# Performance work log

Hardware: AMD Instinct MI355X
Metric: run time of the kernel (lower is better)

Reference implementation:

```python
import jax, jax.numpy as jnp
import numpy as np

N_NODES = 50000


def gcn_conv(x, edge_index, W, b, n_nodes):
    # PyG GCNConv: add self-loops, symmetric normalization, linear, scatter-add.
    src, dst = edge_index[0], edge_index[1]
    loops = jnp.arange(n_nodes, dtype=src.dtype)
    src = jnp.concatenate([src, loops])
    dst = jnp.concatenate([dst, loops])
    # linear transform first (PyG order), reduces scatter width when out < in
    h = x @ W  # [N, out]
    deg = jax.ops.segment_sum(jnp.ones_like(dst, dtype=h.dtype), dst, num_segments=n_nodes)
    dinv = jnp.where(deg > 0, jax.lax.rsqrt(deg), 0.0)
    norm = dinv[src] * dinv[dst]  # [E+N]
    msgs = h[src] * norm[:, None]  # gather + scale, [E+N, out]
    out = jax.ops.segment_sum(msgs, dst, num_segments=n_nodes)  # scatter-add
    return out + b


def setup_inputs() -> dict:
    key = jax.random.key(0)
    k1, k2, k3, k4 = jax.random.split(key, 4)
    in_c, hid_c, out_c = 256, 128, 64
    n_edges = 800000
    features = jax.random.normal(k1, (N_NODES, in_c), dtype=jnp.float32)
    edge_index = jax.random.randint(k2, (2, n_edges), 0, N_NODES, dtype=jnp.int64)
    W1 = jax.random.normal(k3, (in_c, hid_c), dtype=jnp.float32) * (1.0 / np.sqrt(in_c))
    b1 = jnp.zeros((hid_c,), dtype=jnp.float32)
    W2 = jax.random.normal(k4, (hid_c, out_c), dtype=jnp.float32) * (1.0 / np.sqrt(hid_c))
    b2 = jnp.zeros((out_c,), dtype=jnp.float32)
    return {"features": features, "edge_index": edge_index, "W1": W1, "b1": b1, "W2": W2, "b2": b2}


def reference(features, edge_index, W1, b1, W2, b2):
    n = features.shape[0]
    x = gcn_conv(features, edge_index, W1, b1, n)
    x = jax.nn.relu(x)
    # dropout p=0.5 is identity at inference
    x = gcn_conv(x, edge_index, W2, b2, n)
    return x
```

## Files before the change

kernel.cpp:

```cpp
#include <hip/hip_runtime.h>

#define THREADS 256
#define SEG 96

typedef _Float16 f16;
typedef f16   f16x8 __attribute__((ext_vector_type(8)));
typedef float f32x4 __attribute__((ext_vector_type(4)));

__global__ void k_zero(unsigned* __restrict__ cnt, int n4){
  int i = blockIdx.x*blockDim.x + threadIdx.x;
  if(i < n4) ((int4*)cnt)[i] = make_int4(0,0,0,0);
}

__global__ void k_build1(const int* __restrict__ ei, unsigned* __restrict__ cnt,
                         int* __restrict__ ssrc, int E, int M){
  const int grp = blockIdx.x & 7;
  const int nb  = blockIdx.x >> 3;
  const int lo  = grp * (M >> 3);
  const int hi  = (grp == 7) ? M : lo + (M >> 3);
  int e = nb*THREADS + threadIdx.x;
  if(e < E){
    int d = ei[E+e];
    if(d >= lo && d < hi){
      int s = ei[e];
      unsigned p = atomicAdd(&cnt[d], 1u);
      if(p < SEG) ssrc[(size_t)d*SEG + p] = s;
    }
  }
}

template<int K, int N>
__global__ void k_gemm1(const float* __restrict__ A, const float* __restrict__ W,
                        const unsigned* __restrict__ cnt, f16* __restrict__ Hh, int M){
  constexpr int BM = 64, BK = 32, BN = N;
  constexpr int AST = 40;
  constexpr int NM = 4, NN = 2;
  constexpr int SKN = BK*BN/THREADS;
  __shared__ f16 Ah[BM*AST], Bh[BN*AST];

  const int tid  = threadIdx.x;
  const int row0 = blockIdx.x*BM;
  const int wc = tid>>6, l = tid&63;
  const int lr = l&15, lk = l>>4;

  const int sar = tid>>2, sak = (tid&3)*8;
  const long long garow = min(row0+sar, M-1);
  const int sc = tid & (BN-1), sk0 = (tid>>7)*SKN;

  f32x4 acc[NM][NN] = {};

  for(int k0 = 0; k0 < K; k0 += BK){
    float avals[8];
    #pragma unroll
    for(int q=0;q<2;q++){
      float4 v = *(const float4*)(A + garow*K + k0 + sak + q*4);
      avals[q*4+0]=v.x; avals[q*4+1]=v.y; avals[q*4+2]=v.z; avals[q*4+3]=v.w;
    }
    float bvals[SKN];
    #pragma unroll
    for(int i=0;i<SKN;i++) bvals[i] = W[(size_t)(k0+sk0+i)*N + sc];

    __syncthreads();

    {
      f16x8 hv;
      #pragma unroll
      for(int j=0;j<8;j++) hv[j] = (f16)avals[j];
      *(f16x8*)&Ah[sar*AST + sak] = hv;
    }
    #pragma unroll
    for(int s=0;s<SKN/8;s++){
      f16x8 hv;
      #pragma unroll
      for(int j=0;j<8;j++) hv[j] = (f16)bvals[s*8+j];
      *(f16x8*)&Bh[sc*AST + sk0 + s*8] = hv;
    }
    __syncthreads();

    f16x8 af[NM], bf[NN];
    #pragma unroll
    for(int m=0;m<NM;m++){
      int r = m*16 + lr;
      af[m] = *(const f16x8*)&Ah[r*AST + lk*8];
    }
    #pragma unroll
    for(int n=0;n<NN;n++){
      int c = wc*32 + n*16 + lr;
      bf[n] = *(const f16x8*)&Bh[c*AST + lk*8];
    }
    #pragma unroll
    for(int m=0;m<NM;m++)
      #pragma unroll
      for(int n=0;n<NN;n++)
        acc[m][n] = __builtin_amdgcn_mfma_f32_16x16x32_f16(af[m], bf[n], acc[m][n], 0,0,0);
  }

  #pragma unroll
  for(int m=0;m<NM;m++){
    int grb = row0 + m*16 + lk*4;
    #pragma unroll
    for(int reg=0;reg<4;reg++){
      int gr = grb + reg;
      if(gr < M){
        float dv = rsqrtf((float)(cnt[gr] + 1u));
        #pragma unroll
        for(int n=0;n<NN;n++){
          int gc = wc*32 + n*16 + lr;
          Hh[(size_t)gr*N + gc] = (f16)(acc[m][n][reg] * dv);
        }
      }
    }
  }
}

template<int K, int N>
__global__ void k_gemm_mfma_f16a(const f16* __restrict__ A, const float* __restrict__ W,
                                 const unsigned* __restrict__ cnt, f16* __restrict__ Hh, int M){
  constexpr int BM = 64, BK = 32, BN = N;
  constexpr int AST = 40;
  constexpr int NM = 4;
  constexpr int SKN = BK*BN/THREADS;
  __shared__ f16 Ah[BM*AST], Bh[BN*AST];

  const int tid  = threadIdx.x;
  const int row0 = blockIdx.x*BM;
  const int wc = tid>>6, l = tid&63;
  const int lr = l&15, lk = l>>4;

  const int sar = tid>>2, sak = (tid&3)*8;
  const long long garow = min(row0+sar, M-1);
  const int sc = tid & (BN-1), sk0 = (tid>>6)*SKN;

  f32x4 acc[NM] = {};

  for(int k0 = 0; k0 < K; k0 += BK){
    f16x8 av = *(const f16x8*)(A + garow*K + k0 + sak);
    float bvals[SKN];
    #pragma unroll
    for(int i=0;i<SKN;i++) bvals[i] = W[(size_t)(k0+sk0+i)*N + sc];

    __syncthreads();

    *(f16x8*)&Ah[sar*AST + sak] = av;
    {
      f16x8 hv;
      #pragma unroll
      for(int j=0;j<8;j++) hv[j] = (f16)bvals[j];
      *(f16x8*)&Bh[sc*AST + sk0] = hv;
    }
    __syncthreads();

    f16x8 af[NM], bf;
    #pragma unroll
    for(int m=0;m<NM;m++){
      int r = m*16 + lr;
      af[m] = *(const f16x8*)&Ah[r*AST + lk*8];
    }
    {
      int c = wc*16 + lr;
      bf = *(const f16x8*)&Bh[c*AST + lk*8];
    }
    #pragma unroll
    for(int m=0;m<NM;m++)
      acc[m] = __builtin_amdgcn_mfma_f32_16x16x32_f16(af[m], bf, acc[m], 0,0,0);
  }

  #pragma unroll
  for(int m=0;m<NM;m++){
    int grb = row0 + m*16 + lk*4;
    #pragma unroll
    for(int reg=0;reg<4;reg++){
      int gr = grb + reg;
      if(gr < M){
        float dv = rsqrtf((float)(cnt[gr] + 1u));
        int gc = wc*16 + lr;
        Hh[(size_t)gr*N + gc] = (f16)(acc[m][reg] * dv);
      }
    }
  }
}

__global__ void k_gather_l1(const unsigned* __restrict__ cnt, const int* __restrict__ ssrc,
                            const f16* __restrict__ g,
                            const float* __restrict__ bias, f16* __restrict__ outh, int M){
  const int w = (blockIdx.x*blockDim.x + threadIdx.x) >> 6;
  const int l = threadIdx.x & 63;
  if(w >= M) return;
  const int q = l>>4, c = l&15;
  const f16x8* g8 = (const f16x8*)g;
  float acc[8] = {0.f,0.f,0.f,0.f,0.f,0.f,0.f,0.f};
  const int ne = min((int)cnt[w], SEG);
  int it = ne >> 2;
  int i = w*SEG + q;
  while(it >= 4){
    int s0 = ssrc[i], s1 = ssrc[i+4], s2 = ssrc[i+8], s3 = ssrc[i+12];
    f16x8 v0 = g8[(size_t)s0*16 + c];
    f16x8 v1 = g8[(size_t)s1*16 + c];
    f16x8 v2 = g8[(size_t)s2*16 + c];
    f16x8 v3 = g8[(size_t)s3*16 + c];
    #pragma unroll
    for(int j=0;j<8;j++)
      acc[j] += ((float)v0[j] + (float)v1[j]) + ((float)v2[j] + (float)v3[j]);
    i += 16; it -= 4;
  }
  while(it){
    int s = ssrc[i];
    f16x8 v = g8[(size_t)s*16 + c];
    #pragma unroll
    for(int j=0;j<8;j++) acc[j] += (float)v[j];
    i += 4; --it;
  }
  if(q < (ne & 3)){
    int s = ssrc[i];
    f16x8 v = g8[(size_t)s*16 + c];
    #pragma unroll
    for(int j=0;j<8;j++) acc[j] += (float)v[j];
  }
  if(q == 0){
    f16x8 v = g8[(size_t)w*16 + c];
    #pragma unroll
    for(int j=0;j<8;j++) acc[j] += (float)v[j];
  }
  #pragma unroll
  for(int j=0;j<8;j++){
    acc[j] += __shfl_xor(acc[j], 16);
    acc[j] += __shfl_xor(acc[j], 32);
  }
  if(q == 0){
    const float dw = rsqrtf((float)(cnt[w] + 1u));
    float4 b0 = ((const float4*)bias)[c*2];
    float4 b1 = ((const float4*)bias)[c*2+1];
    f16x8 o;
    o[0] = (f16)fmaxf(fmaf(acc[0], dw, b0.x), 0.f);
    o[1] = (f16)fmaxf(fmaf(acc[1], dw, b0.y), 0.f);
    o[2] = (f16)fmaxf(fmaf(acc[2], dw, b0.z), 0.f);
    o[3] = (f16)fmaxf(fmaf(acc[3], dw, b0.w), 0.f);
    o[4] = (f16)fmaxf(fmaf(acc[4], dw, b1.x), 0.f);
    o[5] = (f16)fmaxf(fmaf(acc[5], dw, b1.y), 0.f);
    o[6] = (f16)fmaxf(fmaf(acc[6], dw, b1.z), 0.f);
    o[7] = (f16)fmaxf(fmaf(acc[7], dw, b1.w), 0.f);
    ((f16x8*)outh)[(size_t)w*16 + c] = o;
  }
}

__global__ void k_gather_l2(const unsigned* __restrict__ cnt, const int* __restrict__ ssrc,
                            const f16* __restrict__ g,
                            const float* __restrict__ bias, float* __restrict__ out, int M){
  const int w = (blockIdx.x*blockDim.x + threadIdx.x) >> 6;
  const int l = threadIdx.x & 63;
  if(w >= M) return;
  const int grp = l>>3, c = l&7;
  const f16x8* g8 = (const f16x8*)g;
  float acc[8] = {0.f,0.f,0.f,0.f,0.f,0.f,0.f,0.f};
  const int ne = min((int)cnt[w], SEG);
  int it = ne >> 3;
  int i = w*SEG + grp;
  while(it >= 2){
    int s0 = ssrc[i], s1 = ssrc[i+8];
    f16x8 v0 = g8[(size_t)s0*8 + c];
    f16x8 v1 = g8[(size_t)s1*8 + c];
    #pragma unroll
    for(int j=0;j<8;j++) acc[j] += (float)v0[j] + (float)v1[j];
    i += 16; it -= 2;
  }
  if(it){
    int s = ssrc[i];
    f16x8 v = g8[(size_t)s*8 + c];
    #pragma unroll
    for(int j=0;j<8;j++) acc[j] += (float)v[j];
    i += 8;
  }
  if(grp < (ne & 7)){
    int s = ssrc[i];
    f16x8 v = g8[(size_t)s*8 + c];
    #pragma unroll
    for(int j=0;j<8;j++) acc[j] += (float)v[j];
  }
  if(grp == 0){
    f16x8 v = g8[(size_t)w*8 + c];
    #pragma unroll
    for(int j=0;j<8;j++) acc[j] += (float)v[j];
  }
  #pragma unroll
  for(int j=0;j<8;j++){
    acc[j] += __shfl_xor(acc[j], 8);
    acc[j] += __shfl_xor(acc[j], 16);
    acc[j] += __shfl_xor(acc[j], 32);
  }
  if(grp == 0){
    const float dw = rsqrtf((float)(cnt[w] + 1u));
    float4 b0 = ((const float4*)bias)[c*2];
    float4 b1 = ((const float4*)bias)[c*2+1];
    float4 o0, o1;
    o0.x = fmaf(acc[0], dw, b0.x);
    o0.y = fmaf(acc[1], dw, b0.y);
    o0.z = fmaf(acc[2], dw, b0.z);
    o0.w = fmaf(acc[3], dw, b0.w);
    o1.x = fmaf(acc[4], dw, b1.x);
    o1.y = fmaf(acc[5], dw, b1.y);
    o1.z = fmaf(acc[6], dw, b1.z);
    o1.w = fmaf(acc[7], dw, b1.w);
    ((float4*)out)[(size_t)w*16 + c*2]     = o0;
    ((float4*)out)[(size_t)w*16 + c*2 + 1] = o1;
  }
}

extern "C" void kernel_launch(void* const* d_in, const int* in_sizes, int n_in,
                              void* d_out, int out_size, void* d_ws, size_t ws_size,
                              hipStream_t stream){
  const float* feat = (const float*)d_in[0];
  const int*   ei   = (const int*)d_in[1];
  const float* W1   = (const float*)d_in[2];
  const float* b1   = (const float*)d_in[3];
  const float* W2   = (const float*)d_in[4];
  const float* b2   = (const float*)d_in[5];
  float* out = (float*)d_out;

  const int M = in_sizes[0] / 256;
  const int E = in_sizes[1] / 2;

  float* ws = (float*)d_ws;
  unsigned* cnt  = (unsigned*)ws;
  int*      ssrc = (int*)(ws + 51200);
  f16*      h1h  = (f16*)(ws + 5000000);
  f16*      o1h  = (f16*)(ws + 8400000);
  f16*      h2h  = h1h;

  const int nbE = (E + THREADS-1)/THREADS;
  const int gemmBlocks = (M + 63)/64;
  const int n4 = (M + 3)/4;

  k_zero<<<(n4 + THREADS-1)/THREADS, THREADS, 0, stream>>>(cnt, n4);
  k_build1<<<nbE*8, THREADS, 0, stream>>>(ei, cnt, ssrc, E, M);

  k_gemm1<256,128><<<gemmBlocks, THREADS, 0, stream>>>(feat, W1, cnt, h1h, M);
  k_gather_l1<<<(M*64 + THREADS-1)/THREADS, THREADS, 0, stream>>>(cnt, ssrc, h1h, b1, o1h, M);

  k_gemm_mfma_f16a<128,64><<<gemmBlocks, THREADS, 0, stream>>>(o1h, W2, cnt, h2h, M);
  k_gather_l2<<<(M*64 + THREADS-1)/THREADS, THREADS, 0, stream>>>(cnt, ssrc, h2h, b2, out, M);
}
```

Measured before the change: 132.2 us.

## Bucket per-node neighbour lists by source-index range for gather locality

Splits each destination's neighbour slots into four sub-buckets keyed by the high bits of the source index, with a separate atomic counter per bucket. The gathers iterate bucket by bucket so concurrent reads target a narrower source region, aiming for better cache hit rates. Degree is recomputed as the sum of the four counters. It risks dropping edges if any bucket exceeds 24 entries, assumes node count fits in four 16K ranges, and increases counter memory and loop overhead.

```diff
diff --git a/kernel.cpp b/kernel.cpp
--- a/kernel.cpp
+++ b/kernel.cpp
@@ -1,18 +1,20 @@
 #include <hip/hip_runtime.h>
 
 #define THREADS 256
-#define SEG 96
+#define NPH 4
+#define SUB 24
+#define SEG (NPH*SUB)
 
 typedef _Float16 f16;
 typedef f16   f16x8 __attribute__((ext_vector_type(8)));
 typedef float f32x4 __attribute__((ext_vector_type(4)));
 
-__global__ void k_zero(unsigned* __restrict__ cnt, int n4){
+__global__ void k_zero(unsigned* __restrict__ cnt4, int n4){
   int i = blockIdx.x*blockDim.x + threadIdx.x;
-  if(i < n4) ((int4*)cnt)[i] = make_int4(0,0,0,0);
-}
-
-__global__ void k_build1(const int* __restrict__ ei, unsigned* __restrict__ cnt,
+  if(i < n4) ((int4*)cnt4)[i] = make_int4(0,0,0,0);
+}
+
+__global__ void k_build1(const int* __restrict__ ei, unsigned* __restrict__ cnt4,
                          int* __restrict__ ssrc, int E, int M){
   const int grp = blockIdx.x & 7;
   const int nb  = blockIdx.x >> 3;
@@ -23,15 +25,21 @@
     int d = ei[E+e];
     if(d >= lo && d < hi){
       int s = ei[e];
-      unsigned p = atomicAdd(&cnt[d], 1u);
-      if(p < SEG) ssrc[(size_t)d*SEG + p] = s;
-    }
-  }
+      int ph = s >> 14;
+      unsigned p = atomicAdd(&cnt4[d*NPH + ph], 1u);
+      if(p < SUB) ssrc[(size_t)d*SEG + ph*SUB + p] = s;
+    }
+  }
+}
+
+__device__ __forceinline__ float deg_rsqrt(const unsigned* cnt4, int node){
+  uint4 cc = ((const uint4*)cnt4)[node];
+  return rsqrtf((float)(cc.x + cc.y + cc.z + cc.w + 1u));
 }
 
 template<int K, int N>
 __global__ void k_gemm1(const float* __restrict__ A, const float* __restrict__ W,
-                        const unsigned* __restrict__ cnt, f16* __restrict__ Hh, int M){
+                        const unsigned* __restrict__ cnt4, f16* __restrict__ Hh, int M){
   constexpr int BM = 64, BK = 32, BN = N;
   constexpr int AST = 40;
   constexpr int NM = 4, NN = 2;
@@ -102,7 +110,7 @@
     for(int reg=0;reg<4;reg++){
       int gr = grb + reg;
       if(gr < M){
-        float dv = rsqrtf((float)(cnt[gr] + 1u));
+        float dv = deg_rsqrt(cnt4, gr);
         #pragma unroll
         for(int n=0;n<NN;n++){
           int gc = wc*32 + n*16 + lr;
@@ -115,7 +123,7 @@
 
 template<int K, int N>
 __global__ void k_gemm_mfma_f16a(const f16* __restrict__ A, const float* __restrict__ W,
-                                 const unsigned* __restrict__ cnt, f16* __restrict__ Hh, int M){
+                                 const unsigned* __restrict__ cnt4, f16* __restrict__ Hh, int M){
   constexpr int BM = 64, BK = 32, BN = N;
   constexpr int AST = 40;
   constexpr int NM = 4;
@@ -172,7 +180,7 @@
     for(int reg=0;reg<4;reg++){
       int gr = grb + reg;
       if(gr < M){
-        float dv = rsqrtf((float)(cnt[gr] + 1u));
+        float dv = deg_rsqrt(cnt4, gr);
         int gc = wc*16 + lr;
         Hh[(size_t)gr*N + gc] = (f16)(acc[m][reg] * dv);
       }
@@ -180,7 +188,7 @@
   }
 }
 
-__global__ void k_gather_l1(const unsigned* __restrict__ cnt, const int* __restrict__ ssrc,
+__global__ void k_gather_l1(const unsigned* __restrict__ cnt4, const int* __restrict__ ssrc,
                             const f16* __restrict__ g,
                             const float* __restrict__ bias, f16* __restrict__ outh, int M){
   const int w = (blockIdx.x*blockDim.x + threadIdx.x) >> 6;
@@ -189,32 +197,35 @@
   const int q = l>>4, c = l&15;
   const f16x8* g8 = (const f16x8*)g;
   float acc[8] = {0.f,0.f,0.f,0.f,0.f,0.f,0.f,0.f};
-  const int ne = min((int)cnt[w], SEG);
-  int it = ne >> 2;
-  int i = w*SEG + q;
-  while(it >= 4){
-    int s0 = ssrc[i], s1 = ssrc[i+4], s2 = ssrc[i+8], s3 = ssrc[i+12];
-    f16x8 v0 = g8[(size_t)s0*16 + c];
-    f16x8 v1 = g8[(size_t)s1*16 + c];
-    f16x8 v2 = g8[(size_t)s2*16 + c];
-    f16x8 v3 = g8[(size_t)s3*16 + c];
-    #pragma unroll
-    for(int j=0;j<8;j++)
-      acc[j] += ((float)v0[j] + (float)v1[j]) + ((float)v2[j] + (float)v3[j]);
-    i += 16; it -= 4;
-  }
-  while(it){
-    int s = ssrc[i];
-    f16x8 v = g8[(size_t)s*16 + c];
-    #pragma unroll
-    for(int j=0;j<8;j++) acc[j] += (float)v[j];
-    i += 4; --it;
-  }
-  if(q < (ne & 3)){
-    int s = ssrc[i];
-    f16x8 v = g8[(size_t)s*16 + c];
-    #pragma unroll
-    for(int j=0;j<8;j++) acc[j] += (float)v[j];
+  const uint4 cc = ((const uint4*)cnt4)[w];
+  const unsigned nep[NPH] = {min(cc.x,(unsigned)SUB), min(cc.y,(unsigned)SUB),
+                             min(cc.z,(unsigned)SUB), min(cc.w,(unsigned)SUB)};
+  #pragma unroll
+  for(int ph=0; ph<NPH; ph++){
+    const int ne = (int)nep[ph];
+    int it = ne >> 2;
+    int i = w*SEG + ph*SUB + q;
+    while(it >= 2){
+      int s0 = ssrc[i], s1 = ssrc[i+4];
+      f16x8 v0 = g8[(size_t)s0*16 + c];
+      f16x8 v1 = g8[(size_t)s1*16 + c];
+      #pragma unroll
+      for(int j=0;j<8;j++) acc[j] += (float)v0[j] + (float)v1[j];
+      i += 8; it -= 2;
+    }
+    if(it){
+      int s = ssrc[i];
+      f16x8 v = g8[(size_t)s*16 + c];
+      #pragma unroll
+      for(int j=0;j<8;j++) acc[j] += (float)v[j];
+      i += 4;
+    }
+    if(q < (ne & 3)){
+      int s = ssrc[i];
+      f16x8 v = g8[(size_t)s*16 + c];
+      #pragma unroll
+      for(int j=0;j<8;j++) acc[j] += (float)v[j];
+    }
   }
   if(q == 0){
     f16x8 v = g8[(size_t)w*16 + c];
@@ -227,7 +238,7 @@
     acc[j] += __shfl_xor(acc[j], 32);
   }
   if(q == 0){
-    const float dw = rsqrtf((float)(cnt[w] + 1u));
+    const float dw = rsqrtf((float)(cc.x + cc.y + cc.z + cc.w + 1u));
     float4 b0 = ((const float4*)bias)[c*2];
     float4 b1 = ((const float4*)bias)[c*2+1];
     f16x8 o;
@@ -243,7 +254,7 @@
   }
 }
 
-__global__ void k_gather_l2(const unsigned* __restrict__ cnt, const int* __restrict__ ssrc,
+__global__ void k_gather_l2(const unsigned* __restrict__ cnt4, const int* __restrict__ ssrc,
                             const f16* __restrict__ g,
                             const float* __restrict__ bias, float* __restrict__ out, int M){
   const int w = (blockIdx.x*blockDim.x + threadIdx.x) >> 6;
@@ -252,29 +263,27 @@
   const int grp = l>>3, c = l&7;
   const f16x8* g8 = (const f16x8*)g;
   float acc[8] = {0.f,0.f,0.f,0.f,0.f,0.f,0.f,0.f};
-  const int ne = min((int)cnt[w], SEG);
-  int it = ne >> 3;
-  int i = w*SEG + grp;
-  while(it >= 2){
-    int s0 = ssrc[i], s1 = ssrc[i+8];
-    f16x8 v0 = g8[(size_t)s0*8 + c];
-    f16x8 v1 = g8[(size_t)s1*8 + c];
-    #pragma unroll
-    for(int j=0;j<8;j++) acc[j] += (float)v0[j] + (float)v1[j];
-    i += 16; it -= 2;
-  }
-  if(it){
-    int s = ssrc[i];
-    f16x8 v = g8[(size_t)s*8 + c];
-    #pragma unroll
-    for(int j=0;j<8;j++) acc[j] += (float)v[j];
-    i += 8;
-  }
-  if(grp < (ne & 7)){
-    int s = ssrc[i];
-    f16x8 v = g8[(size_t)s*8 + c];
-    #pragma unroll
-    for(int j=0;j<8;j++) acc[j] += (float)v[j];
+  const uint4 cc = ((const uint4*)cnt4)[w];
+  const unsigned nep[NPH] = {min(cc.x,(unsigned)SUB), min(cc.y,(unsigned)SUB),
+                             min(cc.z,(unsigned)SUB), min(cc.w,(unsigned)SUB)};
+  #pragma unroll
+  for(int ph=0; ph<NPH; ph++){
+    const int ne = (int)nep[ph];
+    int it = ne >> 3;
+    int i = w*SEG + ph*SUB + grp;
+    while(it){
+      int s = ssrc[i];
+      f16x8 v = g8[(size_t)s*8 + c];
+      #pragma unroll
+      for(int j=0;j<8;j++) acc[j] += (float)v[j];
+      i += 8; --it;
+    }
+    if(grp < (ne & 7)){
+      int s = ssrc[i];
+      f16x8 v = g8[(size_t)s*8 + c];
+      #pragma unroll
+      for(int j=0;j<8;j++) acc[j] += (float)v[j];
+    }
   }
   if(grp == 0){
     f16x8 v = g8[(size_t)w*8 + c];
@@ -288,7 +297,7 @@
     acc[j] += __shfl_xor(acc[j], 32);
   }
   if(grp == 0){
-    const float dw = rsqrtf((float)(cnt[w] + 1u));
+    const float dw = rsqrtf((float)(cc.x + cc.y + cc.z + cc.w + 1u));
     float4 b0 = ((const float4*)bias)[c*2];
     float4 b1 = ((const float4*)bias)[c*2+1];
     float4 o0, o1;
@@ -320,22 +329,22 @@
   const int E = in_sizes[1] / 2;
 
   float* ws = (float*)d_ws;
-  unsigned* cnt  = (unsigned*)ws;
-  int*      ssrc = (int*)(ws + 51200);
-  f16*      h1h  = (f16*)(ws + 5000000);
-  f16*      o1h  = (f16*)(ws + 8400000);
+  unsigned* cnt4 = (unsigned*)ws;
+  int*      ssrc = (int*)(ws + 204800);
+  f16*      h1h  = (f16*)(ws + 5004800);
+  f16*      o1h  = (f16*)(ws + 8204800);
   f16*      h2h  = h1h;
 
   const int nbE = (E + THREADS-1)/THREADS;
   const int gemmBlocks = (M + 63)/64;
-  const int n4 = (M + 3)/4;
-
-  k_zero<<<(n4 + THREADS-1)/THREADS, THREADS, 0, stream>>>(cnt, n4);
-  k_build1<<<nbE*8, THREADS, 0, stream>>>(ei, cnt, ssrc, E, M);
-
-  k_gemm1<256,128><<<gemmBlocks, THREADS, 0, stream>>>(feat, W1, cnt, h1h, M);
-  k_gather_l1<<<(M*64 + THREADS-1)/THREADS, THREADS, 0, stream>>>(cnt, ssrc, h1h, b1, o1h, M);
-
-  k_gemm_mfma_f16a<128,64><<<gemmBlocks, THREADS, 0, stream>>>(o1h, W2, cnt, h2h, M);
-  k_gather_l2<<<(M*64 + THREADS-1)/THREADS, THREADS, 0, stream>>>(cnt, ssrc, h2h, b2, out, M);
-}
+  const int n4 = M;
+
+  k_zero<<<(n4 + THREADS-1)/THREADS, THREADS, 0, stream>>>(cnt4, n4);
+  k_build1<<<nbE*8, THREADS, 0, stream>>>(ei, cnt4, ssrc, E, M);
+
+  k_gemm1<256,128><<<gemmBlocks, THREADS, 0, stream>>>(feat, W1, cnt4, h1h, M);
+  k_gather_l1<<<(M*64 + THREADS-1)/THREADS, THREADS, 0, stream>>>(cnt4, ssrc, h1h, b1, o1h, M);
+
+  k_gemm_mfma_f16a<128,64><<<gemmBlocks, THREADS, 0, stream>>>(o1h, W2, cnt4, h2h, M);
+  k_gather_l2<<<(M*64 + THREADS-1)/THREADS, THREADS, 0, stream>>>(cnt4, ssrc, h2h, b2, out, M);
+}
```

Result: slower. 147.2 us (+11.4%).

## Fuse CSR build with layer-1 GEMM, move source normalization into gather

Applied to the files above, without the earlier changes.

The edge-bucketing build kernel and the first GEMM now run as one launch, with the first blocks doing the atomic bucketing and the rest doing the GEMM. This is possible because the GEMM no longer scales rows by the source degree and so does not depend on the counts. The layer-1 gather instead reads cnt[s] per neighbor and applies rsqrt as an FMA weight. The goal is to overlap the atomic-bound build with the compute-bound GEMM and save a launch, at the cost of an extra dependent count load per edge and a shallower unroll in the gather.

```diff
diff --git a/kernel.cpp b/kernel.cpp
--- a/kernel.cpp
+++ b/kernel.cpp
@@ -12,34 +12,37 @@
   if(i < n4) ((int4*)cnt)[i] = make_int4(0,0,0,0);
 }
 
-__global__ void k_build1(const int* __restrict__ ei, unsigned* __restrict__ cnt,
-                         int* __restrict__ ssrc, int E, int M){
-  const int grp = blockIdx.x & 7;
-  const int nb  = blockIdx.x >> 3;
-  const int lo  = grp * (M >> 3);
-  const int hi  = (grp == 7) ? M : lo + (M >> 3);
-  int e = nb*THREADS + threadIdx.x;
-  if(e < E){
-    int d = ei[E+e];
-    if(d >= lo && d < hi){
-      int s = ei[e];
-      unsigned p = atomicAdd(&cnt[d], 1u);
-      if(p < SEG) ssrc[(size_t)d*SEG + p] = s;
-    }
-  }
-}
-
 template<int K, int N>
-__global__ void k_gemm1(const float* __restrict__ A, const float* __restrict__ W,
-                        const unsigned* __restrict__ cnt, f16* __restrict__ Hh, int M){
+__global__ void k_build_gemm1(const int* __restrict__ ei, unsigned* __restrict__ cnt,
+                              int* __restrict__ ssrc, int E, int M,
+                              const float* __restrict__ A, const float* __restrict__ W,
+                              f16* __restrict__ Hh, int buildBlocks){
   constexpr int BM = 64, BK = 32, BN = N;
   constexpr int AST = 40;
   constexpr int NM = 4, NN = 2;
   constexpr int SKN = BK*BN/THREADS;
   __shared__ f16 Ah[BM*AST], Bh[BN*AST];
 
+  if((int)blockIdx.x < buildBlocks){
+    const int grp = blockIdx.x & 7;
+    const int nb  = blockIdx.x >> 3;
+    const int lo  = grp * (M >> 3);
+    const int hi  = (grp == 7) ? M : lo + (M >> 3);
+    int e = nb*THREADS + threadIdx.x;
+    if(e < E){
+      int d = ei[E+e];
+      if(d >= lo && d < hi){
+        int s = ei[e];
+        unsigned p = atomicAdd(&cnt[d], 1u);
+        if(p < SEG) ssrc[(size_t)d*SEG + p] = s;
+      }
+    }
+    return;
+  }
+
+  const int bx   = (int)blockIdx.x - buildBlocks;
   const int tid  = threadIdx.x;
-  const int row0 = blockIdx.x*BM;
+  const int row0 = bx*BM;
   const int wc = tid>>6, l = tid&63;
   const int lr = l&15, lk = l>>4;
 
@@ -102,11 +105,10 @@
     for(int reg=0;reg<4;reg++){
       int gr = grb + reg;
       if(gr < M){
-        float dv = rsqrtf((float)(cnt[gr] + 1u));
         #pragma unroll
         for(int n=0;n<NN;n++){
           int gc = wc*32 + n*16 + lr;
-          Hh[(size_t)gr*N + gc] = (f16)(acc[m][n][reg] * dv);
+          Hh[(size_t)gr*N + gc] = (f16)(acc[m][n][reg]);
         }
       }
     }
@@ -192,34 +194,39 @@
   const int ne = min((int)cnt[w], SEG);
   int it = ne >> 2;
   int i = w*SEG + q;
-  while(it >= 4){
-    int s0 = ssrc[i], s1 = ssrc[i+4], s2 = ssrc[i+8], s3 = ssrc[i+12];
+  while(it >= 2){
+    int s0 = ssrc[i], s1 = ssrc[i+4];
+    float d0 = rsqrtf((float)(cnt[s0] + 1u));
+    float d1 = rsqrtf((float)(cnt[s1] + 1u));
     f16x8 v0 = g8[(size_t)s0*16 + c];
     f16x8 v1 = g8[(size_t)s1*16 + c];
-    f16x8 v2 = g8[(size_t)s2*16 + c];
-    f16x8 v3 = g8[(size_t)s3*16 + c];
-    #pragma unroll
-    for(int j=0;j<8;j++)
-      acc[j] += ((float)v0[j] + (float)v1[j]) + ((float)v2[j] + (float)v3[j]);
-    i += 16; it -= 4;
-  }
-  while(it){
+    #pragma unroll
+    for(int j=0;j<8;j++){
+      acc[j] = fmaf((float)v0[j], d0, acc[j]);
+      acc[j] = fmaf((float)v1[j], d1, acc[j]);
+    }
+    i += 8; it -= 2;
+  }
+  if(it){
     int s = ssrc[i];
+    float ds = rsqrtf((float)(cnt[s] + 1u));
     f16x8 v = g8[(size_t)s*16 + c];
     #pragma unroll
-    for(int j=0;j<8;j++) acc[j] += (float)v[j];
-    i += 4; --it;
+    for(int j=0;j<8;j++) acc[j] = fmaf((float)v[j], ds, acc[j]);
+    i += 4;
   }
   if(q < (ne & 3)){
     int s = ssrc[i];
+    float ds = rsqrtf((float)(cnt[s] + 1u));
     f16x8 v = g8[(size_t)s*16 + c];
     #pragma unroll
-    for(int j=0;j<8;j++) acc[j] += (float)v[j];
-  }
+    for(int j=0;j<8;j++) acc[j] = fmaf((float)v[j], ds, acc[j]);
+  }
+  const float dw = rsqrtf((float)(cnt[w] + 1u));
   if(q == 0){
     f16x8 v = g8[(size_t)w*16 + c];
     #pragma unroll
-    for(int j=0;j<8;j++) acc[j] += (float)v[j];
+    for(int j=0;j<8;j++) acc[j] = fmaf((float)v[j], dw, acc[j]);
   }
   #pragma unroll
   for(int j=0;j<8;j++){
@@ -227,7 +234,6 @@
     acc[j] += __shfl_xor(acc[j], 32);
   }
   if(q == 0){
-    const float dw = rsqrtf((float)(cnt[w] + 1u));
     float4 b0 = ((const float4*)bias)[c*2];
     float4 b1 = ((const float4*)bias)[c*2+1];
     f16x8 o;
@@ -327,13 +333,15 @@
   f16*      h2h  = h1h;
 
   const int nbE = (E + THREADS-1)/THREADS;
+  const int buildBlocks = nbE*8;
   const int gemmBlocks = (M + 63)/64;
   const int n4 = (M + 3)/4;
 
   k_zero<<<(n4 + THREADS-1)/THREADS, THREADS, 0, stream>>>(cnt, n4);
-  k_build1<<<nbE*8, THREADS, 0, stream>>>(ei, cnt, ssrc, E, M);
-
-  k_gemm1<256,128><<<gemmBlocks, THREADS, 0, stream>>>(feat, W1, cnt, h1h, M);
+
+  k_build_gemm1<256,128><<<buildBlocks + gemmBlocks, THREADS, 0, stream>>>(
+      ei, cnt, ssrc, E, M, feat, W1, h1h, buildBlocks);
+
   k_gather_l1<<<(M*64 + THREADS-1)/THREADS, THREADS, 0, stream>>>(cnt, ssrc, h1h, b1, o1h, M);
 
   k_gemm_mfma_f16a<128,64><<<gemmBlocks, THREADS, 0, stream>>>(o1h, W2, cnt, h2h, M);
```

Measured after the change: 129.9 us. About the same (-1.7%).
